# Optimization experiments

Hardware: AMD Instinct MI355X
Metric: run time of the kernel (lower is better)

## Reference

```python
import jax, jax.numpy as jnp
import numpy as np

EPS = 1e-10


def setup_inputs() -> dict:
    key = jax.random.key(0)
    ks = jax.random.split(key, 8)
    b, s, m, r, n = 2, 2048, 1024, 64, 16
    u = jax.random.normal(ks[0], (b, s, m), dtype=jnp.float32)
    delta = jax.random.normal(ks[1], (b, s, r), dtype=jnp.float32)
    dt_proj_w = jax.random.normal(ks[2], (m, r), dtype=jnp.float32) * 0.02
    dt_proj_b = jax.random.normal(ks[3], (m,), dtype=jnp.float32) * 0.02
    # A_log ~ Uniform(-3, -1) as in nn.init.uniform_(self.A_log, -3.0, -1.0)
    A_log = jax.random.uniform(ks[4], (n, m), dtype=jnp.float32, minval=-3.0, maxval=-1.0)
    D_skip = jnp.ones((m,), dtype=jnp.float32)
    # xavier_uniform with gain=0.1 on [n, m]
    bound = 0.1 * np.sqrt(6.0 / (n + m))
    B_proj_w = jax.random.uniform(ks[5], (n, m), dtype=jnp.float32, minval=-bound, maxval=bound)
    C_proj_w = jax.random.uniform(ks[6], (n, m), dtype=jnp.float32, minval=-bound, maxval=bound)
    return {"u": u, "delta": delta, "dt_proj_w": dt_proj_w, "dt_proj_b": dt_proj_b,
            "A_log": A_log, "D_skip": D_skip, "B_proj_w": B_proj_w, "C_proj_w": C_proj_w}


def reference(u, delta, dt_proj_w, dt_proj_b, A_log, D_skip, B_proj_w, C_proj_w):
    # u: [b, s, m]; delta: [b, s, r]
    dt = jax.nn.softplus(jnp.einsum('bsr,mr->bsm', delta, dt_proj_w) + dt_proj_b)
    dt = jnp.clip(dt, 1e-6, 10.0)                      # [b, s, m]
    A = jnp.clip(-jnp.exp(A_log), -10.0, -1e-6)        # [n, m]
    B = jnp.einsum('bsm,nm->bsn', u, B_proj_w)         # [b, s, n]
    C = jnp.einsum('bsm,nm->bsn', u, C_proj_w)         # [b, s, n]

    # associative-scan path (seq_len > 256), math as in _associative_scan:
    # h_t = exp(cumsum_t log(dA)) * cumsum_t (dB_u / dA)
    dA = jnp.exp(dt[:, :, None, :] * A[None, None])    # [b, s, n, m]
    dA_c = jnp.clip(dA, EPS, None)
    dBu = dt[:, :, None, :] * B[..., None] * u[:, :, None, :]  # [b, s, n, m]
    A_cum = jnp.exp(jnp.cumsum(jnp.log(dA_c), axis=1))
    h = A_cum * jnp.cumsum(dBu / dA_c, axis=1)          # [b, s, n, m]
    y = jnp.einsum('bsnm,bsn->bsm', h, C)               # contract state dim

    out = y + u * D_skip
    out = jnp.clip(out, -10000.0, 10000.0)
    bad = jnp.any(~jnp.isfinite(out))
    return jnp.where(bad, jnp.zeros_like(u), out)
```

## Files before the change

### kernel.cpp

```cpp
#include <hip/hip_runtime.h>
#include <math.h>

#define B_ 2
#define S_ 2048
#define M_ 1024
#define R_ 64
#define N_ 16
#define NC 64
#define CH 32
#define LOG2E 1.44269504088896f

#define DT_OFF  0
#define AGG_OFF 4194304
#define BWT_OFF 8388608
#define CWT_OFF 8404992
#define PB_OFF  8421376
#define PC_OFF  8552448

__global__ __launch_bounds__(256) void k_dt(const float* __restrict__ delta,
                                            const float* __restrict__ Wdt,
                                            const float* __restrict__ bdt,
                                            const float* __restrict__ Bw,
                                            const float* __restrict__ Cw,
                                            float* __restrict__ dt,
                                            float* __restrict__ BwT,
                                            float* __restrict__ CwT) {
    int bid = blockIdx.y * 4 + blockIdx.x;
    if (threadIdx.x < 8) {
        int idx = bid * 8 + threadIdx.x;
        int mt = idx >> 4, nt = idx & 15;
        BwT[idx] = Bw[nt * M_ + mt];
        CwT[idx] = Cw[nt * M_ + mt];
    }
    int m    = blockIdx.x * 256 + threadIdx.x;
    int row0 = blockIdx.y * 8;
    float w[R_];
    const float4* W4 = reinterpret_cast<const float4*>(Wdt + (size_t)m * R_);
#pragma unroll
    for (int i = 0; i < R_ / 4; ++i) {
        float4 v = W4[i];
        w[4*i] = v.x; w[4*i+1] = v.y; w[4*i+2] = v.z; w[4*i+3] = v.w;
    }
    float bias = bdt[m];
#pragma unroll 1
    for (int r = 0; r < 8; ++r) {
        int bs = row0 + r;
        const float* dr = delta + (size_t)bs * R_;
        float acc = bias;
#pragma unroll
        for (int k = 0; k < R_; ++k) acc = fmaf(dr[k], w[k], acc);
        float sp = fmaxf(acc, 0.f) + log1pf(expf(-fabsf(acc)));
        sp = fminf(fmaxf(sp, 1e-6f), 10.0f);
        dt[(size_t)bs * M_ + m] = sp;
    }
}

__global__ __launch_bounds__(256) void k_bc_partial(const float* __restrict__ u,
                                                    const float* __restrict__ BwT,
                                                    const float* __restrict__ CwT,
                                                    float* __restrict__ pB,
                                                    float* __restrict__ pC) {
    __shared__ float uLds[16 * 516];
    int r0 = blockIdx.x * 16;
    int k0 = blockIdx.y * 512;
    for (int i = threadIdx.x; i < 2048; i += 256) {
        int r = i >> 7, kq = i & 127;
        float4 v = *reinterpret_cast<const float4*>(&u[(size_t)(r0 + r) * M_ + k0 + kq * 4]);
        *reinterpret_cast<float4*>(&uLds[r * 516 + kq * 4]) = v;
    }
    __syncthreads();
    int r = threadIdx.x >> 4, n = threadIdx.x & 15;
    const float4* u4 = reinterpret_cast<const float4*>(uLds + r * 516);
    float accB = 0.f, accC = 0.f;
#pragma unroll 4
    for (int k4 = 0; k4 < 128; ++k4) {
        float4 uv = u4[k4];
        int kb = k0 + k4 * 4;
        accB = fmaf(uv.x, BwT[(kb+0)*16 + n], accB);
        accB = fmaf(uv.y, BwT[(kb+1)*16 + n], accB);
        accB = fmaf(uv.z, BwT[(kb+2)*16 + n], accB);
        accB = fmaf(uv.w, BwT[(kb+3)*16 + n], accB);
        accC = fmaf(uv.x, CwT[(kb+0)*16 + n], accC);
        accC = fmaf(uv.y, CwT[(kb+1)*16 + n], accC);
        accC = fmaf(uv.z, CwT[(kb+2)*16 + n], accC);
        accC = fmaf(uv.w, CwT[(kb+3)*16 + n], accC);
    }
    size_t o = (size_t)blockIdx.y * 65536 + (size_t)(r0 + r) * 16 + n;
    pB[o] = accB;
    pC[o] = accC;
}

__global__ __launch_bounds__(256, 8) void k_pass1(const float* __restrict__ dt,
                                                  const float* __restrict__ u,
                                                  const float* __restrict__ pB,
                                                  const float* __restrict__ A_log,
                                                  float* __restrict__ Agg) {
    __shared__ float ldsDt[CH * 64], ldsU[CH * 64], ldsB[CH * 16];
    const int m0 = blockIdx.x * 64, c = blockIdx.y, b = blockIdx.z;
    const int s0 = c * CH;
    const int tid = threadIdx.x;
    for (int i = tid; i < 512; i += 256) {
        int s = i >> 4, mq = (i & 15) * 4;
        size_t off = ((size_t)(b * S_ + s0 + s)) * M_ + m0 + mq;
        *reinterpret_cast<float4*>(&ldsDt[s * 64 + mq]) = *reinterpret_cast<const float4*>(&dt[off]);
        *reinterpret_cast<float4*>(&ldsU [s * 64 + mq]) = *reinterpret_cast<const float4*>(&u[off]);
    }
    {
        size_t base = (size_t)(b * S_ + s0) * N_;
        for (int i = tid; i < CH * 16; i += 256)
            ldsB[i] = pB[base + i] + pB[65536 + base + i];
    }
    __syncthreads();
    const int lane = tid & 63, wave = tid >> 6;
    const int ml = wave * 16 + (lane & 15);
    const int m  = m0 + ml;
    const int n0 = (lane >> 4) * 4;
    float Aa2[4], S[4] = {0,0,0,0};
    float T = 0.f;
#pragma unroll
    for (int j = 0; j < 4; ++j) {
        float a = -expf(A_log[(size_t)(n0 + j) * M_ + m]);
        Aa2[j] = fminf(fmaxf(a, -10.f), -1e-6f) * LOG2E;
    }
    for (int s = 0; s < CH; ++s) {
        float dtv = ldsDt[s * 64 + ml];
        float uv  = ldsU [s * 64 + ml];
        float du  = dtv * uv;
        T += dtv;
        float4 bv = *reinterpret_cast<const float4*>(&ldsB[s * 16 + n0]);
        float bb[4] = {bv.x, bv.y, bv.z, bv.w};
#pragma unroll
        for (int j = 0; j < 4; ++j) {
            float em = exp2f(-dtv * Aa2[j]);
            S[j] = fmaf(du * bb[j], em, S[j]);
        }
    }
    float g[4], h[4];
#pragma unroll
    for (int j = 0; j < 4; ++j) {
        g[j] = exp2f(Aa2[j] * T);
        h[j] = g[j] * S[j];
    }
    float* dst = Agg + ((size_t)(b * NC + c) * M_ + m) * 32 + n0 * 2;
    *reinterpret_cast<float4*>(dst)     = make_float4(g[0], h[0], g[1], h[1]);
    *reinterpret_cast<float4*>(dst + 4) = make_float4(g[2], h[2], g[3], h[3]);
}

__global__ __launch_bounds__(64) void k_pass2(float* __restrict__ Agg) {
    const int idx = blockIdx.x * 64 + threadIdx.x;
    const int n = idx & 15;
    const int m = (idx >> 4) & 1023;
    const int b = idx >> 14;
    float* p = Agg + ((size_t)(b * NC) * M_ + m) * 32 + n * 2;
    float grun = 1.f, hrun = 0.f;
#pragma unroll 1
    for (int c0 = 0; c0 < NC; c0 += 8) {
        float2 v[8];
#pragma unroll
        for (int t = 0; t < 8; ++t)
            v[t] = *reinterpret_cast<const float2*>(p + (size_t)(c0 + t) * (M_ * 32));
#pragma unroll
        for (int t = 0; t < 8; ++t) {
            *reinterpret_cast<float2*>(p + (size_t)(c0 + t) * (M_ * 32)) =
                make_float2(grun, hrun);
            hrun = fmaf(v[t].x, hrun, grun * v[t].y);
            grun *= v[t].x;
        }
    }
}

__global__ __launch_bounds__(256, 8) void k_pass3(const float* __restrict__ dt,
                                                  const float* __restrict__ u,
                                                  const float* __restrict__ pB,
                                                  const float* __restrict__ pC,
                                                  const float* __restrict__ A_log,
                                                  const float* __restrict__ Dskip,
                                                  const float* __restrict__ Agg,
                                                  float* __restrict__ out) {
    __shared__ float ldsDt[CH * 64], ldsU[CH * 64], ldsB[CH * 16], ldsC[CH * 16];
    const int m0 = blockIdx.x * 64, c = blockIdx.y, b = blockIdx.z;
    const int s0 = c * CH;
    const int tid = threadIdx.x;
    for (int i = tid; i < 512; i += 256) {
        int s = i >> 4, mq = (i & 15) * 4;
        size_t off = ((size_t)(b * S_ + s0 + s)) * M_ + m0 + mq;
        *reinterpret_cast<float4*>(&ldsDt[s * 64 + mq]) = *reinterpret_cast<const float4*>(&dt[off]);
        *reinterpret_cast<float4*>(&ldsU [s * 64 + mq]) = *reinterpret_cast<const float4*>(&u[off]);
    }
    {
        size_t base = (size_t)(b * S_ + s0) * N_;
        for (int i = tid; i < CH * 16; i += 256) {
            ldsB[i] = pB[base + i] + pB[65536 + base + i];
            ldsC[i] = pC[base + i] + pC[65536 + base + i];
        }
    }
    __syncthreads();
    const int lane = tid & 63, wave = tid >> 6;
    const int ml = wave * 16 + (lane & 15);
    const int m  = m0 + ml;
    const int ng = lane >> 4, n0 = ng * 4;
    float Aa2[4], g[4], h[4];
    {
        const float* ini = Agg + ((size_t)(b * NC + c) * M_ + m) * 32 + n0 * 2;
        float4 q0 = *reinterpret_cast<const float4*>(ini);
        float4 q1 = *reinterpret_cast<const float4*>(ini + 4);
        g[0] = q0.x; h[0] = q0.y; g[1] = q0.z; h[1] = q0.w;
        g[2] = q1.x; h[2] = q1.y; g[3] = q1.z; h[3] = q1.w;
    }
#pragma unroll
    for (int j = 0; j < 4; ++j) {
        float a = -expf(A_log[(size_t)(n0 + j) * M_ + m]);
        Aa2[j] = fminf(fmaxf(a, -10.f), -1e-6f) * LOG2E;
    }
    const float Dm = Dskip[m];
    for (int s = 0; s < CH; ++s) {
        float dtv = ldsDt[s * 64 + ml];
        float uv  = ldsU [s * 64 + ml];
        float du  = dtv * uv;
        float4 bv = *reinterpret_cast<const float4*>(&ldsB[s * 16 + n0]);
        float4 cv = *reinterpret_cast<const float4*>(&ldsC[s * 16 + n0]);
        float bb[4] = {bv.x, bv.y, bv.z, bv.w};
        float cc[4] = {cv.x, cv.y, cv.z, cv.w};
        float y = 0.f;
#pragma unroll
        for (int j = 0; j < 4; ++j) {
            float ea = exp2f(dtv * Aa2[j]);
            h[j] = fmaf(ea, h[j], g[j] * (du * bb[j]));
            g[j] *= ea;
            y = fmaf(h[j], cc[j], y);
        }
        y += __shfl_xor(y, 16, 64);
        y += __shfl_xor(y, 32, 64);
        if (ng == 0) {
            float o = y + uv * Dm;
            o = fminf(fmaxf(o, -10000.f), 10000.f);
            out[((size_t)(b * S_ + s0 + s)) * M_ + m] = o;
        }
    }
}

extern "C" void kernel_launch(void* const* d_in, const int* in_sizes, int n_in,
                              void* d_out, int out_size, void* d_ws, size_t ws_size,
                              hipStream_t stream) {
    const float* u     = (const float*)d_in[0];
    const float* delta = (const float*)d_in[1];
    const float* Wdt   = (const float*)d_in[2];
    const float* bdt   = (const float*)d_in[3];
    const float* A_log = (const float*)d_in[4];
    const float* Dski  = (const float*)d_in[5];
    const float* Bw    = (const float*)d_in[6];
    const float* Cw    = (const float*)d_in[7];
    float* out = (float*)d_out;
    float* ws  = (float*)d_ws;

    float* dt  = ws + DT_OFF;
    float* Agg = ws + AGG_OFF;
    float* BwT = ws + BWT_OFF;
    float* CwT = ws + CWT_OFF;
    float* pB  = ws + PB_OFF;
    float* pC  = ws + PC_OFF;

    k_dt<<<dim3(4, 512), 256, 0, stream>>>(delta, Wdt, bdt, Bw, Cw, dt, BwT, CwT);
    k_bc_partial<<<dim3(256, 2), 256, 0, stream>>>(u, BwT, CwT, pB, pC);
    k_pass1<<<dim3(16, NC, B_), 256, 0, stream>>>(dt, u, pB, A_log, Agg);
    k_pass2<<<512, 64, 0, stream>>>(Agg);
    k_pass3<<<dim3(16, NC, B_), 256, 0, stream>>>(dt, u, pB, pC, A_log, Dski, Agg, out);
}
```

Measured before the change: 114.5 us.

## Fold chunk-prefix scan into pass3 and drop separate pass2 kernel

Removes the standalone inter-chunk scan kernel. Each pass3 block now combines the per-chunk aggregates of all preceding chunks itself, overlapping that work with its LDS staging by moving the barrier later. Pass1 switches from the exp(-dt*A) cumulative-sum form to the direct recurrence, which avoids overflow-prone positive exponents. Launch-bounds occupancy hints are also dropped. The trade-off is redundant work: later chunks re-read up to 63 aggregates per thread, which adds quadratic global traffic in place of one kernel launch and one sequential pass.

```diff
diff --git a/kernel.cpp b/kernel.cpp
--- a/kernel.cpp
+++ b/kernel.cpp
@@ -90,11 +90,11 @@
     pC[o] = accC;
 }
 
-__global__ __launch_bounds__(256, 8) void k_pass1(const float* __restrict__ dt,
-                                                  const float* __restrict__ u,
-                                                  const float* __restrict__ pB,
-                                                  const float* __restrict__ A_log,
-                                                  float* __restrict__ Agg) {
+__global__ __launch_bounds__(256) void k_pass1(const float* __restrict__ dt,
+                                               const float* __restrict__ u,
+                                               const float* __restrict__ pB,
+                                               const float* __restrict__ A_log,
+                                               float* __restrict__ Agg) {
     __shared__ float ldsDt[CH * 64], ldsU[CH * 64], ldsB[CH * 16];
     const int m0 = blockIdx.x * 64, c = blockIdx.y, b = blockIdx.z;
     const int s0 = c * CH;
@@ -115,8 +115,7 @@
     const int ml = wave * 16 + (lane & 15);
     const int m  = m0 + ml;
     const int n0 = (lane >> 4) * 4;
-    float Aa2[4], S[4] = {0,0,0,0};
-    float T = 0.f;
+    float Aa2[4], h[4] = {0,0,0,0}, g[4] = {1.f,1.f,1.f,1.f};
 #pragma unroll
     for (int j = 0; j < 4; ++j) {
         float a = -expf(A_log[(size_t)(n0 + j) * M_ + m]);
@@ -126,57 +125,28 @@
         float dtv = ldsDt[s * 64 + ml];
         float uv  = ldsU [s * 64 + ml];
         float du  = dtv * uv;
-        T += dtv;
         float4 bv = *reinterpret_cast<const float4*>(&ldsB[s * 16 + n0]);
         float bb[4] = {bv.x, bv.y, bv.z, bv.w};
 #pragma unroll
         for (int j = 0; j < 4; ++j) {
-            float em = exp2f(-dtv * Aa2[j]);
-            S[j] = fmaf(du * bb[j], em, S[j]);
-        }
-    }
-    float g[4], h[4];
-#pragma unroll
-    for (int j = 0; j < 4; ++j) {
-        g[j] = exp2f(Aa2[j] * T);
-        h[j] = g[j] * S[j];
+            float ea = exp2f(dtv * Aa2[j]);
+            h[j] = fmaf(ea, h[j], g[j] * (du * bb[j]));
+            g[j] *= ea;
+        }
     }
     float* dst = Agg + ((size_t)(b * NC + c) * M_ + m) * 32 + n0 * 2;
     *reinterpret_cast<float4*>(dst)     = make_float4(g[0], h[0], g[1], h[1]);
     *reinterpret_cast<float4*>(dst + 4) = make_float4(g[2], h[2], g[3], h[3]);
 }
 
-__global__ __launch_bounds__(64) void k_pass2(float* __restrict__ Agg) {
-    const int idx = blockIdx.x * 64 + threadIdx.x;
-    const int n = idx & 15;
-    const int m = (idx >> 4) & 1023;
-    const int b = idx >> 14;
-    float* p = Agg + ((size_t)(b * NC) * M_ + m) * 32 + n * 2;
-    float grun = 1.f, hrun = 0.f;
-#pragma unroll 1
-    for (int c0 = 0; c0 < NC; c0 += 8) {
-        float2 v[8];
-#pragma unroll
-        for (int t = 0; t < 8; ++t)
-            v[t] = *reinterpret_cast<const float2*>(p + (size_t)(c0 + t) * (M_ * 32));
-#pragma unroll
-        for (int t = 0; t < 8; ++t) {
-            *reinterpret_cast<float2*>(p + (size_t)(c0 + t) * (M_ * 32)) =
-                make_float2(grun, hrun);
-            hrun = fmaf(v[t].x, hrun, grun * v[t].y);
-            grun *= v[t].x;
-        }
-    }
-}
-
-__global__ __launch_bounds__(256, 8) void k_pass3(const float* __restrict__ dt,
-                                                  const float* __restrict__ u,
-                                                  const float* __restrict__ pB,
-                                                  const float* __restrict__ pC,
-                                                  const float* __restrict__ A_log,
-                                                  const float* __restrict__ Dskip,
-                                                  const float* __restrict__ Agg,
-                                                  float* __restrict__ out) {
+__global__ __launch_bounds__(256) void k_pass3(const float* __restrict__ dt,
+                                               const float* __restrict__ u,
+                                               const float* __restrict__ pB,
+                                               const float* __restrict__ pC,
+                                               const float* __restrict__ A_log,
+                                               const float* __restrict__ Dskip,
+                                               const float* __restrict__ Agg,
+                                               float* __restrict__ out) {
     __shared__ float ldsDt[CH * 64], ldsU[CH * 64], ldsB[CH * 16], ldsC[CH * 16];
     const int m0 = blockIdx.x * 64, c = blockIdx.y, b = blockIdx.z;
     const int s0 = c * CH;
@@ -194,25 +164,50 @@
             ldsC[i] = pC[base + i] + pC[65536 + base + i];
         }
     }
-    __syncthreads();
     const int lane = tid & 63, wave = tid >> 6;
     const int ml = wave * 16 + (lane & 15);
     const int m  = m0 + ml;
     const int ng = lane >> 4, n0 = ng * 4;
-    float Aa2[4], g[4], h[4];
+
+    float g[4] = {1.f,1.f,1.f,1.f}, h[4] = {0.f,0.f,0.f,0.f};
     {
-        const float* ini = Agg + ((size_t)(b * NC + c) * M_ + m) * 32 + n0 * 2;
-        float4 q0 = *reinterpret_cast<const float4*>(ini);
-        float4 q1 = *reinterpret_cast<const float4*>(ini + 4);
-        g[0] = q0.x; h[0] = q0.y; g[1] = q0.z; h[1] = q0.w;
-        g[2] = q1.x; h[2] = q1.y; g[3] = q1.z; h[3] = q1.w;
-    }
+        const float* aggB = Agg + ((size_t)(b * NC) * M_ + m) * 32 + n0 * 2;
+        const size_t cstride = (size_t)M_ * 32;
+        int cp = 0;
+        for (; cp + 4 <= c; cp += 4) {
+            float4 q[8];
+#pragma unroll
+            for (int t = 0; t < 4; ++t) {
+                q[2*t]   = *reinterpret_cast<const float4*>(aggB + (size_t)(cp + t) * cstride);
+                q[2*t+1] = *reinterpret_cast<const float4*>(aggB + (size_t)(cp + t) * cstride + 4);
+            }
+#pragma unroll
+            for (int t = 0; t < 4; ++t) {
+                float4 a0 = q[2*t], a1 = q[2*t+1];
+                h[0] = fmaf(a0.x, h[0], g[0] * a0.y); g[0] *= a0.x;
+                h[1] = fmaf(a0.z, h[1], g[1] * a0.w); g[1] *= a0.z;
+                h[2] = fmaf(a1.x, h[2], g[2] * a1.y); g[2] *= a1.x;
+                h[3] = fmaf(a1.z, h[3], g[3] * a1.w); g[3] *= a1.z;
+            }
+        }
+        for (; cp < c; ++cp) {
+            float4 a0 = *reinterpret_cast<const float4*>(aggB + (size_t)cp * cstride);
+            float4 a1 = *reinterpret_cast<const float4*>(aggB + (size_t)cp * cstride + 4);
+            h[0] = fmaf(a0.x, h[0], g[0] * a0.y); g[0] *= a0.x;
+            h[1] = fmaf(a0.z, h[1], g[1] * a0.w); g[1] *= a0.z;
+            h[2] = fmaf(a1.x, h[2], g[2] * a1.y); g[2] *= a1.x;
+            h[3] = fmaf(a1.z, h[3], g[3] * a1.w); g[3] *= a1.z;
+        }
+    }
+    float Aa2[4];
 #pragma unroll
     for (int j = 0; j < 4; ++j) {
         float a = -expf(A_log[(size_t)(n0 + j) * M_ + m]);
         Aa2[j] = fminf(fmaxf(a, -10.f), -1e-6f) * LOG2E;
     }
     const float Dm = Dskip[m];
+    __syncthreads();
+
     for (int s = 0; s < CH; ++s) {
         float dtv = ldsDt[s * 64 + ml];
         float uv  = ldsU [s * 64 + ml];
@@ -263,6 +258,5 @@
     k_dt<<<dim3(4, 512), 256, 0, stream>>>(delta, Wdt, bdt, Bw, Cw, dt, BwT, CwT);
     k_bc_partial<<<dim3(256, 2), 256, 0, stream>>>(u, BwT, CwT, pB, pC);
     k_pass1<<<dim3(16, NC, B_), 256, 0, stream>>>(dt, u, pB, A_log, Agg);
-    k_pass2<<<512, 64, 0, stream>>>(Agg);
     k_pass3<<<dim3(16, NC, B_), 256, 0, stream>>>(dt, u, pB, pC, A_log, Dski, Agg, out);
 }
```

Result: slower. 162.1 us (+41.6%).
